# Kernel tuning notes

Measured on AMD Instinct MI355X. Metric: run time of the kernel, lower is better.

The kernel has to match this reference:

```python
import jax, jax.numpy as jnp
import numpy as np

N_GRAPHS = 1000
P = 300                 # nodes per ring graph
N = N_GRAPHS * P        # 300000 nodes
IN_DIM = 2
HID = 128
OUT_DIM = 2


def _ring_edges():
    idx = jnp.arange(N)
    g = idx // P
    pos = idx % P
    nxt = g * P + (pos + 1) % P
    src = jnp.concatenate([idx, nxt])
    dst = jnp.concatenate([nxt, idx])
    return jnp.stack([src, dst]), g


def setup_inputs() -> dict:
    key = jax.random.key(0)
    ks = jax.random.split(key, 11)
    edge_index, batch = _ring_edges()
    x = jax.random.normal(ks[0], (N, IN_DIM), jnp.float32)

    def glorot(k, fan_in, fan_out):
        lim = np.sqrt(6.0 / (fan_in + fan_out)).astype(np.float32)
        return jax.random.uniform(k, (fan_in, fan_out), jnp.float32, -lim, lim)

    return {
        "x": x,
        "edge_index": edge_index,
        "batch": batch,
        "W1": glorot(ks[1], IN_DIM, HID), "b1": jnp.zeros((HID,), jnp.float32),
        "W2": glorot(ks[2], HID, HID),    "b2": jnp.zeros((HID,), jnp.float32),
        "W3": glorot(ks[3], HID, HID),    "b3": jnp.zeros((HID,), jnp.float32),
        "fw1": glorot(ks[4], HID, HID),   "fb1": jnp.zeros((HID,), jnp.float32),
        "fw2": glorot(ks[5], HID, OUT_DIM), "fb2": jnp.zeros((OUT_DIM,), jnp.float32),
    }


def _gcn_conv(x, W, b, src, dst, norm):
    h = x @ W                              # [N, out]
    msg = h[src] * norm[:, None]           # gather + per-edge scale
    agg = jax.ops.segment_sum(msg, dst, num_segments=N)  # scatter-add
    return agg + b


def reference(x, edge_index, batch, W1, b1, W2, b2, W3, b3, fw1, fb1, fw2, fb2):
    loop = jnp.arange(N)
    src = jnp.concatenate([edge_index[0], loop])
    dst = jnp.concatenate([edge_index[1], loop])
    deg = jax.ops.segment_sum(jnp.ones_like(dst, jnp.float32), dst, num_segments=N)
    dis = jax.lax.rsqrt(deg)               # deg >= 1 due to self-loops
    norm = dis[src] * dis[dst]             # per-edge normalization

    h = jax.nn.relu(_gcn_conv(x, W1, b1, src, dst, norm))
    h = jax.nn.relu(_gcn_conv(h, W2, b2, src, dst, norm))
    h = jax.nn.relu(_gcn_conv(h, W3, b3, src, dst, norm))

    # global mean pool per graph
    sums = jax.ops.segment_sum(h, batch, num_segments=N_GRAPHS)
    cnts = jax.ops.segment_sum(jnp.ones((N,), jnp.float32), batch, num_segments=N_GRAPHS)
    pooled = sums / cnts[:, None]

    out = jax.nn.relu(pooled @ fw1 + fb1)
    out = out @ fw2 + fb2
    return out
```

## Files before the change

### kernel.cpp

```cpp
#include <hip/hip_runtime.h>
#include <hip/hip_bf16.h>
#include <stdint.h>

#define P    300
#define HID  128
#define NG   1000
#define NTL  19

typedef __attribute__((ext_vector_type(8))) short bf16x8;
typedef __attribute__((ext_vector_type(4))) short bf16x4;
typedef __attribute__((ext_vector_type(4))) float f32x4;

__device__ short g_wsw[2 * HID * HID];

__device__ __forceinline__ short f2bf(float f) {
    union { float f; uint32_t u; } v; v.f = f;
    uint32_t r = v.u + 0x7fffu + ((v.u >> 16) & 1u);
    return (short)(r >> 16);
}
__device__ __forceinline__ uint32_t pkbf2(float a, float b) {
    union { __hip_bfloat162 h; uint32_t u; } cv;
    cv.h = __float22bfloat162_rn(float2{a, b});
    return cv.u;
}

__device__ __forceinline__ f32x4 mfma16(bf16x4 a, bf16x4 b, f32x4 c) {
#if __has_builtin(__builtin_amdgcn_mfma_f32_16x16x16bf16_1k)
    return __builtin_amdgcn_mfma_f32_16x16x16bf16_1k(a, b, c, 0, 0, 0);
#else
    asm("v_mfma_f32_16x16x16_bf16 %0, %1, %2, %0" : "+v"(c) : "v"(a), "v"(b));
    return c;
#endif
}

__global__ __launch_bounds__(256) void k_prep(const float* __restrict__ W2,
                                              const float* __restrict__ W3) {
    int b = blockIdx.x;
    const float* W = (b < 8) ? W2 : W3;
    short* dst = g_wsw + ((b < 8) ? 0 : HID * HID);
    int t    = (b & 7) * 256 + threadIdx.x;
    int fkey = t >> 4;
    int kc   = t & 15;
    bf16x8 o;
    #pragma unroll
    for (int j = 0; j < 8; ++j)
        o[j] = f2bf(W[(kc * 8 + j) * HID + fkey]);
    *(bf16x8*)&dst[(fkey * 16 + (kc ^ (fkey & 15))) * 8] = o;
}

template<int POOL>
__device__ __forceinline__ void run_pass(short* __restrict__ buf,
                                         const short* __restrict__ wbase,
                                         const float* __restrict__ bias,
                                         float* __restrict__ pool, int tid) {
    const int lane = tid & 63, wv = tid >> 6, q = lane >> 4, lm = lane & 15;
    const int fkey = wv * 16 + lm;
    bf16x8 wf[4];
    #pragma unroll
    for (int kk = 0; kk < 4; ++kk)
        wf[kk] = *(const bf16x8*)&wbase[(fkey * 16 + ((4 * kk + q) ^ lm)) * 8];
    const float biaf = bias[fkey];
    const int kcs = fkey >> 3, offs = fkey & 7;

    const short ONE = (short)0x3F80;
    bf16x4 Sb = {0, 0, 0, 0}, Sp = {0, 0, 0, 0}, Sn = {0, 0, 0, 0},
           Swa = {0, 0, 0, 0}, Swb = {0, 0, 0, 0};
    #pragma unroll
    for (int j = 0; j < 4; ++j) {
        const int k = 4 * q + j;
        if (((lm & 3) == 0 && k == lm - 1) || ((lm & 3) == 3 && k == lm + 1))
            Sb[j] = ONE;
        if (lm == 0  && k == 15) Sp[j]  = ONE;
        if (lm == 15 && k == 0 ) Sn[j]  = ONE;
        if (lm == 11 && k == 0 ) Swa[j] = ONE;
        if (lm == 0  && k == 11) Swb[j] = ONE;
    }

    float psum = 0.f;

    auto mfma_tile = [&](int t, f32x4 &G) {
        const short* tb = buf + t * 2048;
        G = f32x4{0.f, 0.f, 0.f, 0.f};
        #pragma unroll
        for (int kk = 0; kk < 4; ++kk) {
            bf16x8 af = *(const bf16x8*)&tb[(lm * 16 + ((4 * kk + q) ^ lm)) * 8];
            G = __builtin_amdgcn_mfma_f32_16x16x32_bf16(af, wf[kk], G, 0, 0, 0);
        }
    };
    auto pack = [&](const f32x4 &G, bf16x4 &d) {
        union { bf16x4 v; uint32_t u[2]; } pk;
        pk.u[0] = pkbf2(G[0], G[1]);
        pk.u[1] = pkbf2(G[2], G[3]);
        d = pk.v;
    };
    auto store_rows = [&](int T, float (&o)[4]) {
        #pragma unroll
        for (int i = 0; i < 4; ++i) {
            int node = T * 16 + q * 4 + i;
            buf[(node * 16 + (kcs ^ (node & 15))) * 8 + offs] = f2bf(o[i]);
        }
    };
    auto accum = [&](float (&o)[4]) { psum += o[0] + o[1] + o[2] + o[3]; };

    auto epi = [&](const f32x4 &E, const bf16x4 &bT, const bf16x4 &bP,
                   const bf16x4 &bN, int wrap, const bf16x4 &bW,
                   float (&o)[4]) {
        f32x4 C = {0.f, 0.f, 0.f, 0.f};
        C = mfma16(Sb, bT, C);
        C = mfma16(Sp, bP, C);
        C = mfma16(Sn, bN, C);
        if (wrap == 1) C = mfma16(Swa, bW, C);
        if (wrap == 2) C = mfma16(Swb, bW, C);
        const float s0 = E[0] + E[1];
        const float s2 = E[2] + E[3];
        float t0 = C[0] + s0;
        float t1 = s0 + E[2];
        float t2 = E[1] + s2;
        float t3 = s2 + C[3];
        float v0 = fmaf(t0, 1.f / 3.f, biaf);
        float v1 = fmaf(t1, 1.f / 3.f, biaf);
        float v2 = fmaf(t2, 1.f / 3.f, biaf);
        float v3 = fmaf(t3, 1.f / 3.f, biaf);
        o[0] = v0 > 0.f ? v0 : 0.f;
        o[1] = v1 > 0.f ? v1 : 0.f;
        o[2] = v2 > 0.f ? v2 : 0.f;
        o[3] = v3 > 0.f ? v3 : 0.f;
    };

    f32x4 G0c, Gp, Ga, Gb;
    bf16x4 bq0, bq1, bqA, bqB, bqC, bqD;

    mfma_tile(0, G0c);
    pack(G0c, bq0);
    bqB = bq0;
    bqA = bq0;
    Gp = G0c;

    for (int j = 1; j <= 9; ++j) {
        mfma_tile(2 * j - 1, Ga); pack(Ga, bqC);
        mfma_tile(2 * j,     Gb); pack(Gb, bqD);
        if (j == 1) bq1 = bqC;
        if (!POOL) __syncthreads();
        if (j > 1) {
            float o[4];
            epi(Gp, bqB, bqA, bqC, 0, bq0, o);
            if (POOL) accum(o); else store_rows(2 * j - 2, o);
        }
        {
            float o[4];
            epi(Ga, bqC, bqB, bqD, 0, bq0, o);
            if (POOL) accum(o); else store_rows(2 * j - 1, o);
        }
        Gp = Gb; bqA = bqC; bqB = bqD;
    }

    {
        float o18[4];
        epi(Gp, bqB, bqA, bq0, 1, bq0, o18);
        if (q < 3) { if (POOL) accum(o18); else store_rows(18, o18); }
        float o0[4];
        epi(G0c, bq0, bqB, bq1, 2, bqB, o0);
        if (POOL) accum(o0); else store_rows(0, o0);
    }

    if (POOL) {
        psum += __shfl_xor(psum, 16, 64);
        psum += __shfl_xor(psum, 32, 64);
        if (q == 0) pool[fkey] = psum;
    }
}

__global__ __launch_bounds__(512, 1) void k_graph(
        const float* __restrict__ x,
        const float* __restrict__ W1,  const float* __restrict__ b1,
        const float* __restrict__ b2v, const float* __restrict__ b3v,
        const float* __restrict__ fw1, const float* __restrict__ fb1,
        const float* __restrict__ fw2, const float* __restrict__ fb2,
        float* __restrict__ out) {
    __shared__ __align__(16) short buf[304 * HID];
    __shared__ __align__(16) float scr[640];
    float* xs    = scr;
    float* pool  = scr;
    float* parts = scr + 128;
    float* s1    = scr + 384;

    const int g = blockIdx.x, tid = threadIdx.x;

    if (tid < 150) *(float4*)&xs[tid * 4] = *(const float4*)&x[g * 600 + tid * 4];
    __syncthreads();

    {
        const int kc1 = tid & 15;
        const int n0  = tid >> 4;
        float w1x[8], w1y[8], b1v[8];
        #pragma unroll
        for (int j = 0; j < 8; ++j) {
            w1x[j] = W1[kc1 * 8 + j];
            w1y[j] = W1[HID + kc1 * 8 + j];
            b1v[j] = b1[kc1 * 8 + j];
        }
        #pragma unroll
        for (int it = 0; it < 10; ++it) {
            int node = it * 32 + n0;
            if (node < 304) {
                uint32_t w[4] = {0u, 0u, 0u, 0u};
                if (node < P) {
                    int prev = (node == 0)     ? P - 1 : node - 1;
                    int next = (node == P - 1) ? 0     : node + 1;
                    float2 xp = *(const float2*)&xs[2 * prev];
                    float2 xc = *(const float2*)&xs[2 * node];
                    float2 xn = *(const float2*)&xs[2 * next];
                    float ax = (xp.x + xc.x + xn.x) * (1.f / 3.f);
                    float ay = (xp.y + xc.y + xn.y) * (1.f / 3.f);
                    #pragma unroll
                    for (int jj = 0; jj < 4; ++jj) {
                        float va = ax * w1x[2*jj]   + ay * w1y[2*jj]   + b1v[2*jj];
                        float vb = ax * w1x[2*jj+1] + ay * w1y[2*jj+1] + b1v[2*jj+1];
                        va = va > 0.f ? va : 0.f;
                        vb = vb > 0.f ? vb : 0.f;
                        w[jj] = pkbf2(va, vb);
                    }
                }
                *(uint4*)&buf[(node * 16 + (kc1 ^ (node & 15))) * 8] =
                    uint4{w[0], w[1], w[2], w[3]};
            }
        }
    }
    __syncthreads();

    run_pass<0>(buf, g_wsw,             b2v, pool, tid);
    __syncthreads();
    run_pass<1>(buf, g_wsw + HID * HID, b3v, pool, tid);
    __syncthreads();

    if (tid < 256) {
        int f = tid & 127, half = tid >> 7;
        float p = 0.f;
        const float* fw1c = fw1 + f;
        #pragma unroll 4
        for (int k = half * 64; k < half * 64 + 64; ++k)
            p += pool[k] * fw1c[k * 128];
        parts[half * 128 + f] = p;
    }
    __syncthreads();
    if (tid < 128) {
        float o1 = fb1[tid] + (parts[tid] + parts[128 + tid]) * (1.0f / 300.0f);
        s1[tid] = o1 > 0.f ? o1 : 0.f;
    }
    __syncthreads();
    if (tid < 128) {
        int o = tid >> 6, ln = tid & 63;
        float v = s1[ln] * fw2[ln * 2 + o] + s1[ln + 64] * fw2[(ln + 64) * 2 + o];
        #pragma unroll
        for (int off = 1; off <= 32; off <<= 1)
            v += __shfl_xor(v, off, 64);
        if (ln == 0) out[g * 2 + o] = v + fb2[o];
    }
}

extern "C" void kernel_launch(void* const* d_in, const int* in_sizes, int n_in,
                              void* d_out, int out_size, void* d_ws, size_t ws_size,
                              hipStream_t stream) {
    const float* x   = (const float*)d_in[0];
    const float* W1  = (const float*)d_in[3];
    const float* b1  = (const float*)d_in[4];
    const float* W2  = (const float*)d_in[5];
    const float* b2  = (const float*)d_in[6];
    const float* W3  = (const float*)d_in[7];
    const float* b3  = (const float*)d_in[8];
    const float* fw1 = (const float*)d_in[9];
    const float* fb1 = (const float*)d_in[10];
    const float* fw2 = (const float*)d_in[11];
    const float* fb2 = (const float*)d_in[12];
    float* out = (float*)d_out;

    k_prep <<<dim3(16), dim3(256), 0, stream>>>(W2, W3);
    k_graph<<<dim3(NG), dim3(512), 0, stream>>>(x, W1, b1, b2, b3,
                                                fw1, fb1, fw2, fb2, out);
}
```

Baseline: 125.8 us.

## Replace MFMA-based neighbor sums with shuffles and restructure tile schedule in two halves

The ring-neighbour contribution was computed with small 16x16x16 MFMAs against selector matrices on bf16-packed tiles. It is now gathered with cross-lane shuffles of the fp32 GEMM results. The per-graph schedule changes from a rolling two-tile loop with a barrier per iteration to two phases: compute the upper tiles plus tile 0, sync, compute the lower tiles while writing the upper outputs, sync, then write the lower outputs. This cuts the barrier count and removes the bf16 packing of neighbours, which also slightly changes rounding. Launch bounds now request two blocks per CU, at the cost of many live f32x4 accumulators that may raise register pressure or cause spills.

```diff
diff --git a/kernel.cpp b/kernel.cpp
--- a/kernel.cpp
+++ b/kernel.cpp
@@ -8,7 +8,6 @@
 #define NTL  19
 
 typedef __attribute__((ext_vector_type(8))) short bf16x8;
-typedef __attribute__((ext_vector_type(4))) short bf16x4;
 typedef __attribute__((ext_vector_type(4))) float f32x4;
 
 __device__ short g_wsw[2 * HID * HID];
@@ -22,15 +21,6 @@
     union { __hip_bfloat162 h; uint32_t u; } cv;
     cv.h = __float22bfloat162_rn(float2{a, b});
     return cv.u;
-}
-
-__device__ __forceinline__ f32x4 mfma16(bf16x4 a, bf16x4 b, f32x4 c) {
-#if __has_builtin(__builtin_amdgcn_mfma_f32_16x16x16bf16_1k)
-    return __builtin_amdgcn_mfma_f32_16x16x16bf16_1k(a, b, c, 0, 0, 0);
-#else
-    asm("v_mfma_f32_16x16x16_bf16 %0, %1, %2, %0" : "+v"(c) : "v"(a), "v"(b));
-    return c;
-#endif
 }
 
 __global__ __launch_bounds__(256) void k_prep(const float* __restrict__ W2,
@@ -48,6 +38,16 @@
     *(bf16x8*)&dst[(fkey * 16 + (kc ^ (fkey & 15))) * 8] = o;
 }
 
+__device__ __forceinline__ void avg_epi(const f32x4 &G, float vp0, float vn3,
+                                        float b, float* o) {
+    o[0] = (vp0  + G[0] + G[1]) * (1.0f / 3.0f) + b;
+    o[1] = (G[0] + G[1] + G[2]) * (1.0f / 3.0f) + b;
+    o[2] = (G[1] + G[2] + G[3]) * (1.0f / 3.0f) + b;
+    o[3] = (G[2] + G[3] + vn3 ) * (1.0f / 3.0f) + b;
+    #pragma unroll
+    for (int i = 0; i < 4; ++i) o[i] = o[i] > 0.f ? o[i] : 0.f;
+}
+
 template<int POOL>
 __device__ __forceinline__ void run_pass(short* __restrict__ buf,
                                          const short* __restrict__ wbase,
@@ -61,20 +61,8 @@
         wf[kk] = *(const bf16x8*)&wbase[(fkey * 16 + ((4 * kk + q) ^ lm)) * 8];
     const float biaf = bias[fkey];
     const int kcs = fkey >> 3, offs = fkey & 7;
-
-    const short ONE = (short)0x3F80;
-    bf16x4 Sb = {0, 0, 0, 0}, Sp = {0, 0, 0, 0}, Sn = {0, 0, 0, 0},
-           Swa = {0, 0, 0, 0}, Swb = {0, 0, 0, 0};
-    #pragma unroll
-    for (int j = 0; j < 4; ++j) {
-        const int k = 4 * q + j;
-        if (((lm & 3) == 0 && k == lm - 1) || ((lm & 3) == 3 && k == lm + 1))
-            Sb[j] = ONE;
-        if (lm == 0  && k == 15) Sp[j]  = ONE;
-        if (lm == 15 && k == 0 ) Sn[j]  = ONE;
-        if (lm == 11 && k == 0 ) Swa[j] = ONE;
-        if (lm == 0  && k == 11) Swb[j] = ONE;
-    }
+    const int sA = (q == 0) ? (48 + lm) : (lane - 16);
+    const int sB = (lane + 16) & 63;
 
     float psum = 0.f;
 
@@ -87,80 +75,77 @@
             G = __builtin_amdgcn_mfma_f32_16x16x32_bf16(af, wf[kk], G, 0, 0, 0);
         }
     };
-    auto pack = [&](const f32x4 &G, bf16x4 &d) {
-        union { bf16x4 v; uint32_t u[2]; } pk;
-        pk.u[0] = pkbf2(G[0], G[1]);
-        pk.u[1] = pkbf2(G[2], G[3]);
-        d = pk.v;
-    };
     auto store_rows = [&](int T, float (&o)[4]) {
-        #pragma unroll
-        for (int i = 0; i < 4; ++i) {
-            int node = T * 16 + q * 4 + i;
-            buf[(node * 16 + (kcs ^ (node & 15))) * 8 + offs] = f2bf(o[i]);
-        }
+        uint32_t u01 = pkbf2(o[0], o[1]);
+        uint32_t u23 = pkbf2(o[2], o[3]);
+        int n0 = T * 16 + q * 4;
+        buf[(n0 * 16       + (kcs ^ ( n0      & 15))) * 8 + offs] = (short)u01;
+        buf[((n0 + 1) * 16 + (kcs ^ ((n0 + 1) & 15))) * 8 + offs] = (short)(u01 >> 16);
+        buf[((n0 + 2) * 16 + (kcs ^ ((n0 + 2) & 15))) * 8 + offs] = (short)u23;
+        buf[((n0 + 3) * 16 + (kcs ^ ((n0 + 3) & 15))) * 8 + offs] = (short)(u23 >> 16);
     };
     auto accum = [&](float (&o)[4]) { psum += o[0] + o[1] + o[2] + o[3]; };
 
-    auto epi = [&](const f32x4 &E, const bf16x4 &bT, const bf16x4 &bP,
-                   const bf16x4 &bN, int wrap, const bf16x4 &bW,
-                   float (&o)[4]) {
-        f32x4 C = {0.f, 0.f, 0.f, 0.f};
-        C = mfma16(Sb, bT, C);
-        C = mfma16(Sp, bP, C);
-        C = mfma16(Sn, bN, C);
-        if (wrap == 1) C = mfma16(Swa, bW, C);
-        if (wrap == 2) C = mfma16(Swb, bW, C);
-        const float s0 = E[0] + E[1];
-        const float s2 = E[2] + E[3];
-        float t0 = C[0] + s0;
-        float t1 = s0 + E[2];
-        float t2 = E[1] + s2;
-        float t3 = s2 + C[3];
-        float v0 = fmaf(t0, 1.f / 3.f, biaf);
-        float v1 = fmaf(t1, 1.f / 3.f, biaf);
-        float v2 = fmaf(t2, 1.f / 3.f, biaf);
-        float v3 = fmaf(t3, 1.f / 3.f, biaf);
-        o[0] = v0 > 0.f ? v0 : 0.f;
-        o[1] = v1 > 0.f ? v1 : 0.f;
-        o[2] = v2 > 0.f ? v2 : 0.f;
-        o[3] = v3 > 0.f ? v3 : 0.f;
+    float c15;
+    auto epi_mid = [&](const f32x4 &E, float N0, float (&o)[4]) {
+        float vA = __shfl(E[3], sA, 64);
+        float vB = __shfl(E[0], sB, 64);
+        float vC = __shfl(N0, lm, 64);
+        float vp0 = (q == 0) ? c15 : vA;
+        float vn3 = (q == 3) ? vC : vB;
+        avg_epi(E, vp0, vn3, biaf, o);
+        c15 = vA;
     };
 
-    f32x4 G0c, Gp, Ga, Gb;
-    bf16x4 bq0, bq1, bqA, bqB, bqC, bqD;
-
-    mfma_tile(0, G0c);
-    pack(G0c, bq0);
-    bqB = bq0;
-    bqA = bq0;
-    Gp = G0c;
-
-    for (int j = 1; j <= 9; ++j) {
-        mfma_tile(2 * j - 1, Ga); pack(Ga, bqC);
-        mfma_tile(2 * j,     Gb); pack(Gb, bqD);
-        if (j == 1) bq1 = bqC;
-        if (!POOL) __syncthreads();
-        if (j > 1) {
+    f32x4 GH[10];
+    f32x4 GL[9];
+
+    #pragma unroll
+    for (int k = 0; k < 9; ++k) mfma_tile(10 + k, GH[k]);
+    mfma_tile(0, GH[9]);
+    if (!POOL) __syncthreads();
+
+    #pragma unroll
+    for (int i = 0; i < 9; ++i) {
+        mfma_tile(9 - i, GL[i]);
+        if (i == 0) c15 = __shfl(GL[0][3], 48 + lm, 64);
+        if (i < 8) {
             float o[4];
-            epi(Gp, bqB, bqA, bqC, 0, bq0, o);
-            if (POOL) accum(o); else store_rows(2 * j - 2, o);
-        }
-        {
-            float o[4];
-            epi(Ga, bqC, bqB, bqD, 0, bq0, o);
-            if (POOL) accum(o); else store_rows(2 * j - 1, o);
-        }
-        Gp = Gb; bqA = bqC; bqB = bqD;
-    }
-
-    {
-        float o18[4];
-        epi(Gp, bqB, bqA, bq0, 1, bq0, o18);
-        if (q < 3) { if (POOL) accum(o18); else store_rows(18, o18); }
-        float o0[4];
-        epi(G0c, bq0, bqB, bq1, 2, bqB, o0);
-        if (POOL) accum(o0); else store_rows(0, o0);
+            epi_mid(GH[i], GH[i + 1][0], o);
+            if (POOL) accum(o); else store_rows(10 + i, o);
+        } else {
+            float o18[4];
+            {
+                float vA = __shfl(GH[8][3], sA, 64);
+                float vB = __shfl(GH[8][0], sB, 64);
+                float vZ = __shfl(GH[9][0], lm, 64);
+                float vp0 = (q == 0) ? c15 : vA;
+                float vn3 = (q == 2) ? vZ : vB;
+                avg_epi(GH[8], vp0, vn3, biaf, o18);
+            }
+            if (q < 3) { if (POOL) accum(o18); else store_rows(18, o18); }
+            float o0[4];
+            {
+                float vA0 = __shfl(GH[9][3], (lane - 16) & 63, 64);
+                float vB0 = __shfl(GH[9][0], sB, 64);
+                float vP  = __shfl(GH[8][3], 32 + lm, 64);
+                float vN  = __shfl(GL[8][0], lm, 64);
+                float vp0 = (q == 0) ? vP : vA0;
+                float vn3 = (q == 3) ? vN : vB0;
+                avg_epi(GH[9], vp0, vn3, biaf, o0);
+            }
+            if (POOL) accum(o0); else store_rows(0, o0);
+        }
+    }
+    if (!POOL) __syncthreads();
+
+    c15 = __shfl(GH[9][3], 48 + lm, 64);
+    #pragma unroll
+    for (int T = 1; T <= 9; ++T) {
+        float o[4];
+        float N0 = (T < 9) ? GL[8 - T][0] : GH[0][0];
+        epi_mid(GL[9 - T], N0, o);
+        if (POOL) accum(o); else store_rows(T, o);
     }
 
     if (POOL) {
@@ -170,7 +155,7 @@
     }
 }
 
-__global__ __launch_bounds__(512, 1) void k_graph(
+__global__ __launch_bounds__(512, 2) void k_graph(
         const float* __restrict__ x,
         const float* __restrict__ W1,  const float* __restrict__ b1,
         const float* __restrict__ b2v, const float* __restrict__ b3v,
```

Measured after the change: 121.6 us (median of 3 runs). -3.4%, faster.
